# Optimization experiments

Measured on AMD Instinct MI355X. Metric: run time of the kernel, lower is better.

The kernel has to match this reference:

```python
import jax, jax.numpy as jnp
import numpy as np

B, S, HID, NH, KCLIP = 2, 1500, 1024, 16, 64
HD = HID // NH  # 64


def setup_inputs() -> dict:
    key = jax.random.key(0)
    ks = jax.random.split(key, 16)
    std = 0.02
    inp = {
        "query": jax.random.normal(ks[0], (B, S, HID), jnp.float32),
        "key": jax.random.normal(ks[1], (B, S, HID), jnp.float32),
        "value": jax.random.normal(ks[2], (B, S, HID), jnp.float32),
        # per-head projection weights, stacked over heads: [NH, HID, HD]
        "Wq": jax.random.normal(ks[3], (NH, HID, HD), jnp.float32) * std,
        "bq": jax.random.normal(ks[4], (NH, HD), jnp.float32) * std,
        "Wk": jax.random.normal(ks[5], (NH, HID, HD), jnp.float32) * std,
        "bk": jax.random.normal(ks[6], (NH, HD), jnp.float32) * std,
        "Wv": jax.random.normal(ks[7], (NH, HID, HD), jnp.float32) * std,
        "bv": jax.random.normal(ks[8], (NH, HD), jnp.float32) * std,
        # Shaw relative-position embedding tables: [2k+1, HD]
        "pe_k": jax.random.normal(ks[9], (2 * KCLIP + 1, HD), jnp.float32) * std,
        "pe_v": jax.random.normal(ks[10], (2 * KCLIP + 1, HD), jnp.float32) * std,
        # output projection (torch Linear stored as x @ W + b here)
        "W_fc": jax.random.normal(ks[11], (HID, HID), jnp.float32) * std,
        "b_fc": jax.random.normal(ks[12], (HID,), jnp.float32) * std,
    }
    return inp


def _rel_bias(pe, length, k_clip):
    idx = jnp.arange(length)
    dist = jnp.clip(idx[None, :] - idx[:, None], -k_clip, k_clip) + k_clip
    return pe[dist]  # [S, S, HD]


def reference(query, key, value, Wq, bq, Wk, bk, Wv, bv, pe_k, pe_v, W_fc, b_fc):
    head_dim = Wq.shape[-1]
    seq = query.shape[1]
    k_clip = (pe_k.shape[0] - 1) // 2

    kb = _rel_bias(pe_k, seq, k_clip)  # [S, S, HD]
    vb = _rel_bias(pe_v, seq, k_clip)  # [S, S, HD]

    # batched per-head projections: [B, NH, S, HD]
    Q = jnp.einsum('bsh,nhd->bnsd', query, Wq) + bq[None, :, None, :]
    K = jnp.einsum('bsh,nhd->bnsd', key, Wk) + bk[None, :, None, :]
    V = jnp.einsum('bsh,nhd->bnsd', value, Wv) + bv[None, :, None, :]

    # content term + Shaw relative-key bias term
    scores = jnp.einsum('bnqd,bnkd->bnqk', Q, K) \
           + jnp.einsum('bnqd,qkd->bnqk', Q, kb)
    scores = scores / jnp.sqrt(jnp.asarray(head_dim, scores.dtype))

    w = jax.nn.softmax(scores, axis=-1)  # [B, NH, S, S]

    out = jnp.einsum('bnqk,bnkd->bnqd', w, V) \
        + jnp.einsum('bnqk,qkd->bnqd', w, vb)

    # concat heads (head order matches ModuleList concatenation)
    hidden = out.transpose(0, 2, 1, 3).reshape(query.shape[0], seq, -1)
    return hidden @ W_fc + b_fc
```

## Files before the change

### kernel.cpp

```cpp
#include <hip/hip_runtime.h>
#include <math.h>

#define B_     2
#define S_     1500
#define HID_   1024
#define NH_    16
#define HD_    64
#define M_     (B_*S_)
#define SP_    1536
#define LOG2E  1.4426950408889634f

typedef short bf16x8 __attribute__((ext_vector_type(8)));
typedef short bf16x4 __attribute__((ext_vector_type(4)));
typedef float f32x4  __attribute__((ext_vector_type(4)));

__device__ __forceinline__ float b2f(short s) {
    unsigned u = ((unsigned)(unsigned short)s) << 16;
    return __uint_as_float(u);
}
__device__ __forceinline__ short f2b(float f) {
    unsigned u = __float_as_uint(f);
    unsigned r = (u + 0x7FFFu + ((u >> 16) & 1u)) >> 16;
    return (short)r;
}
__device__ __forceinline__ void gload16(const short* src, short* lds) {
    __builtin_amdgcn_global_load_lds(
        (const __attribute__((address_space(1))) void*)src,
        (__attribute__((address_space(3))) void*)lds, 16, 0, 0);
}

__global__ __launch_bounds__(256) void cvt_act3(
    const float* __restrict__ q, const float* __restrict__ k,
    const float* __restrict__ v, short* __restrict__ oq,
    short* __restrict__ ok, short* __restrict__ ov)
{
    const float* src = blockIdx.y == 0 ? q : blockIdx.y == 1 ? k : v;
    short* dst       = blockIdx.y == 0 ? oq : blockIdx.y == 1 ? ok : ov;
    int i = blockIdx.x * 256 + threadIdx.x;
    const float4* p = (const float4*)(src + (size_t)i * 8);
    float4 a = p[0], b = p[1];
    bf16x8 o;
    o[0]=f2b(a.x); o[1]=f2b(a.y); o[2]=f2b(a.z); o[3]=f2b(a.w);
    o[4]=f2b(b.x); o[5]=f2b(b.y); o[6]=f2b(b.z); o[7]=f2b(b.w);
    *(bf16x8*)(dst + (size_t)i * 8) = o;
}

__global__ __launch_bounds__(256) void prep_w(
    const float* __restrict__ Wq, const float* __restrict__ Wk,
    const float* __restrict__ Wv, const float* __restrict__ Wfc,
    const float* __restrict__ pe_k, const float* __restrict__ pe_v,
    short* __restrict__ Wqt, short* __restrict__ Wkt, short* __restrict__ Wvt,
    short* __restrict__ Wfh, short* __restrict__ Wfl,
    short* __restrict__ pe_kb, short* __restrict__ pe_vt)
{
    int z = blockIdx.x, tid = threadIdx.x;
    if (z == 1024) {
        for (int s = tid; s < 144 * 64; s += 256) {
            int j = s >> 6, d = s & 63;
            pe_kb[s] = (j < 129) ? f2b(pe_k[j * 64 + d]) : (short)0;
        }
        for (int s = tid; s < 64 * 160; s += 256) {
            int d = s / 160, j = s - d * 160;
            pe_vt[s] = (j < 129) ? f2b(pe_v[j * 64 + d]) : (short)0;
        }
        return;
    }
    __shared__ float T[64][65];
    const float* src; short* dhi; short* dlo = nullptr;
    int C, c0, r0; float scale = 1.f;
    if (z < 768) {
        int widx = z >> 8, rem = z & 255;
        int h = rem >> 4, rt = rem & 15;
        src = (widx == 0 ? Wq : widx == 1 ? Wk : Wv) + (size_t)h * 1024 * 64;
        dhi = (widx == 0 ? Wqt : widx == 1 ? Wkt : Wvt) + (size_t)h * 64 * 1024;
        scale = (widx == 0) ? 0.125f * LOG2E : 1.0f;
        C = 64; c0 = 0; r0 = rt * 64;
    } else {
        int idx = z - 768;
        src = Wfc; dhi = Wfh; dlo = Wfl;
        C = 1024; c0 = (idx >> 4) * 64; r0 = (idx & 15) * 64;
    }
#pragma unroll
    for (int i = 0; i < 4; ++i) {
        int slot = tid + i * 256;
        int r = slot >> 4, cg = (slot & 15) * 4;
        float4 v = *(const float4*)(src + (size_t)(r0 + r) * C + c0 + cg);
        T[r][cg+0] = v.x*scale; T[r][cg+1] = v.y*scale;
        T[r][cg+2] = v.z*scale; T[r][cg+3] = v.w*scale;
    }
    __syncthreads();
#pragma unroll
    for (int i = 0; i < 16; ++i) {
        int slot = tid + i * 256;
        int c = slot >> 6, r = slot & 63;
        float v = T[r][c];
        short hi = f2b(v);
        size_t o = (size_t)(c0 + c) * 1024 + r0 + r;
        dhi[o] = hi;
        if (dlo) dlo[o] = f2b(v - b2f(hi));
    }
}

__device__ __forceinline__ void gemm_core(
    const short* __restrict__ Ahi, const short* __restrict__ Alo,
    const short* __restrict__ Bhi, const short* __restrict__ Blo,
    int kIters, int m0, int n0, short* As, short* Bs, f32x4 (&acc)[4][4])
{
    const int tid = threadIdx.x, w = tid >> 6, lane = tid & 63;
    const int l15 = lane & 15, lr4 = lane >> 4;
    const int wr = w >> 1, wc = w & 1;

    for (int it = 0; it < kIters; ++it) {
        int kt = it * 64;
        int seg = kt >> 10, kk0 = kt & 1023;
        const short* Aseg = (seg == 1) ? Alo : Ahi;
        const short* Bseg = (seg == 2) ? Blo : Bhi;
        __syncthreads();
#pragma unroll
        for (int c = 0; c < 4; ++c) {
            int slot = (w * 4 + c) * 64 + lane;
            int r = slot >> 3, cb = slot & 7;
            int sm = m0 + r; sm = sm < M_ ? sm : M_ - 1;
            gload16(Aseg + (size_t)sm * 1024 + kk0 + ((cb ^ (r & 7)) * 8),
                    As + (size_t)(w * 4 + c) * 512);
            gload16(Bseg + (size_t)(n0 + r) * 1024 + kk0 + ((cb ^ (r & 7)) * 8),
                    Bs + (size_t)(w * 4 + c) * 512);
        }
        __syncthreads();
#pragma unroll
        for (int kh = 0; kh < 2; ++kh) {
            bf16x8 aF[4], bF[4];
#pragma unroll
            for (int mi = 0; mi < 4; ++mi) {
                int r = wr * 64 + mi * 16 + l15;
                aF[mi] = *(const bf16x8*)(As + r * 64 + (((kh*4+lr4) ^ (r & 7)) * 8));
            }
#pragma unroll
            for (int ni = 0; ni < 4; ++ni) {
                int r = wc * 64 + ni * 16 + l15;
                bF[ni] = *(const bf16x8*)(Bs + r * 64 + (((kh*4+lr4) ^ (r & 7)) * 8));
            }
#pragma unroll
            for (int mi = 0; mi < 4; ++mi)
#pragma unroll
                for (int ni = 0; ni < 4; ++ni)
                    acc[mi][ni] = __builtin_amdgcn_mfma_f32_16x16x32_bf16(
                        aF[mi], bF[ni], acc[mi][ni], 0, 0, 0);
        }
    }
}

__global__ __launch_bounds__(256) void gemm_qkv(
    const short* __restrict__ qb, const short* __restrict__ kb,
    const short* __restrict__ vb, const short* __restrict__ Wqt,
    const short* __restrict__ Wkt, const short* __restrict__ Wvt,
    const float* __restrict__ bq, const float* __restrict__ bk,
    const float* __restrict__ bv,
    short* __restrict__ Qp, short* __restrict__ Kp, short* __restrict__ Vp)
{
    __shared__ short As[128 * 64];
    __shared__ short Bs[128 * 64];
    const int z = blockIdx.z;
    const short* A  = z == 0 ? qb : z == 1 ? kb : vb;
    const short* Bw = z == 0 ? Wqt : z == 1 ? Wkt : Wvt;
    const float* bias = z == 0 ? bq : z == 1 ? bk : bv;
    const float bscale = z == 0 ? 0.125f * LOG2E : 1.0f;
    short* out = z == 0 ? Qp : z == 1 ? Kp : Vp;
    const int m0 = blockIdx.x * 128, n0 = blockIdx.y * 128;

    f32x4 zf = {0.f,0.f,0.f,0.f};
    f32x4 acc[4][4];
#pragma unroll
    for (int i = 0; i < 4; ++i)
#pragma unroll
        for (int j = 0; j < 4; ++j) acc[i][j] = zf;

    gemm_core(A, A, Bw, Bw, 16, m0, n0, As, Bs, acc);

    const int tid = threadIdx.x, w = tid >> 6, lane = tid & 63;
    const int l15 = lane & 15, lr4 = lane >> 4;
    const int wr = w >> 1, wc = w & 1;
#pragma unroll
    for (int mi = 0; mi < 4; ++mi)
#pragma unroll
        for (int rr = 0; rr < 4; ++rr) {
            int m = m0 + wr * 64 + mi * 16 + lr4 * 4 + rr;
            if (m >= M_) continue;
            int b = m / S_, s = m - b * S_;
#pragma unroll
            for (int ni = 0; ni < 4; ++ni) {
                int n = n0 + wc * 64 + ni * 16 + l15;
                float v = acc[mi][ni][rr] + bias[n] * bscale;
                int h = n >> 6, d = n & 63;
                out[(((size_t)(b * NH_ + h)) * S_ + s) * HD_ + d] = f2b(v);
            }
        }
}

__global__ __launch_bounds__(256) void gemm_fc(
    const short* __restrict__ Ahi, const short* __restrict__ Alo,
    const short* __restrict__ Bhi, const short* __restrict__ Blo,
    const float* __restrict__ bias, float* __restrict__ out)
{
    __shared__ short As[128 * 64];
    __shared__ short Bs[128 * 64];
    const int m0 = blockIdx.x * 128, n0 = blockIdx.y * 128;
    f32x4 zf = {0.f,0.f,0.f,0.f};
    f32x4 acc[4][4];
#pragma unroll
    for (int i = 0; i < 4; ++i)
#pragma unroll
        for (int j = 0; j < 4; ++j) acc[i][j] = zf;

    gemm_core(Ahi, Alo, Bhi, Blo, 32, m0, n0, As, Bs, acc);

    const int tid = threadIdx.x, w = tid >> 6, lane = tid & 63;
    const int l15 = lane & 15, lr4 = lane >> 4;
    const int wr = w >> 1, wc = w & 1;
#pragma unroll
    for (int mi = 0; mi < 4; ++mi)
#pragma unroll
        for (int rr = 0; rr < 4; ++rr) {
            int m = m0 + wr * 64 + mi * 16 + lr4 * 4 + rr;
            if (m >= M_) continue;
#pragma unroll
            for (int ni = 0; ni < 4; ++ni) {
                int n = n0 + wc * 64 + ni * 16 + l15;
                out[(size_t)m * 1024 + n] = acc[mi][ni][rr] + bias[n];
            }
        }
}

__global__ __launch_bounds__(256) void vtrans(
    const short* __restrict__ Vp, short* __restrict__ Vtg)
{
    __shared__ short T[64][72];
    const int bh = blockIdx.y, s0 = blockIdx.x * 64, tid = threadIdx.x;
    const size_t kv = (size_t)bh * S_ * 64;
#pragma unroll
    for (int i = 0; i < 2; ++i) {
        int slot = tid + i * 256;
        int r = slot >> 3, cb = slot & 7;
        int ss = s0 + r; ss = ss < S_ ? ss : S_ - 1;
        bf16x8 v = *(const bf16x8*)(Vp + kv + (size_t)ss * 64 + cb * 8);
        *(bf16x8*)(&T[r][cb * 8]) = v;
    }
    __syncthreads();
#pragma unroll
    for (int i = 0; i < 2; ++i) {
        int slot = tid + i * 256;
        int d = slot >> 3, cg = slot & 7;
        bf16x8 v;
#pragma unroll
        for (int j = 0; j < 8; ++j) {
            int kk = 32 * (cg >> 2) + ((j >> 2) & 1) * 16 + (cg & 3) * 4 + (j & 3);
            v[j] = T[kk][d];
        }
        *(bf16x8*)(Vtg + ((size_t)bh * 64 + d) * SP_ + s0 + cg * 8) = v;
    }
}

__global__ __launch_bounds__(256) void attn_mfma(
    const short* __restrict__ Qb, const short* __restrict__ Kb,
    const short* __restrict__ Vtg, const short* __restrict__ pe_kb,
    const short* __restrict__ pe_vt,
    short* __restrict__ hid_hi, short* __restrict__ hid_lo)
{
    __shared__ short Kc[128 * 64];
    __shared__ short Vt[64 * 128];
    __shared__ short qpe[64 * 144];
    __shared__ short wsm[64 * 160];

    const int tid = threadIdx.x, w = tid >> 6, lane = tid & 63;
    const int l15 = lane & 15, lr4 = lane >> 4;
    const int lg = (blockIdx.x & 7) * 96 + (blockIdx.x >> 3);
    const int bh = lg / 24, bx = lg - bh * 24;
    const int q0 = bx * 64;
    const int qw = q0 + w * 16;
    const int myq = qw + l15;
    const int myrow = w * 16 + l15;
    const size_t kv  = (size_t)bh * S_ * HD_;
    const size_t vtb = (size_t)bh * 64 * SP_;

    {
        short ini = f2b(-1e30f);
        bf16x8 iv;
#pragma unroll
        for (int i = 0; i < 8; ++i) iv[i] = ini;
        short* base = wsm + w * 16 * 160;
#pragma unroll
        for (int i = 0; i < 5; ++i)
            *(bf16x8*)(base + (size_t)(i * 64 + lane) * 8) = iv;
    }
#pragma unroll
    for (int cc = 0; cc < 2; ++cc) {
        int slot = (w * 2 + cc) * 64 + lane;
        int r = slot >> 3, cb = slot & 7;
        int sq = q0 + r; sq = sq < S_ ? sq : S_ - 1;
        gload16(Qb + kv + (size_t)sq * 64 + ((cb ^ (r & 7)) * 8),
                Kc + (size_t)(w * 2 + cc) * 512);
    }
    __syncthreads();

    bf16x8 qA[2];
    {
        int r = myrow;
        qA[0] = *(const bf16x8*)(Kc + r * 64 + ((lr4 ^ (r & 7)) * 8));
        qA[1] = *(const bf16x8*)(Kc + r * 64 + (((4 + lr4) ^ (r & 7)) * 8));
    }

    f32x4 zf = {0.f,0.f,0.f,0.f};
#pragma unroll
    for (int jt = 0; jt < 9; ++jt) {
        f32x4 a = zf;
#pragma unroll
        for (int kh = 0; kh < 2; ++kh) {
            bf16x8 pf = *(const bf16x8*)(pe_kb + (size_t)(jt * 16 + l15) * 64 + kh * 32 + lr4 * 8);
            a = __builtin_amdgcn_mfma_f32_16x16x32_bf16(pf, qA[kh], a, 0, 0, 0);
        }
        bf16x4 pk;
#pragma unroll
        for (int rr = 0; rr < 4; ++rr) pk[rr] = f2b(a[rr]);
        *(bf16x4*)(qpe + (size_t)myrow * 144 + jt * 16 + lr4 * 4) = pk;
    }
    const float qpe0   = b2f(qpe[myrow * 144 + 0]);
    const float qpe128 = b2f(qpe[myrow * 144 + 128]);
    __syncthreads();

    float m = -1e30f, s0s = 0.f, s1s = 0.f;
    f32x4 o[4];
#pragma unroll
    for (int t = 0; t < 4; ++t) o[t] = zf;

    for (int c = 0; c < 12; ++c) {
        const int kc = c * 128;
#pragma unroll
        for (int cc = 0; cc < 4; ++cc) {
            int slot = (w * 4 + cc) * 64 + lane;
            int rK = slot >> 3, cbK = slot & 7;
            int sk = kc + rK; sk = sk < S_ ? sk : S_ - 1;
            gload16(Kb + kv + (size_t)sk * 64 + ((cbK ^ (rK & 7)) * 8),
                    Kc + (size_t)(w * 4 + cc) * 512);
            int rV = slot >> 4, cbV = slot & 15;
            gload16(Vtg + vtb + (size_t)rV * SP_ + kc + ((cbV ^ (rV & 7)) * 8),
                    Vt + (size_t)(w * 4 + cc) * 512);
        }
        __syncthreads();

        __builtin_amdgcn_s_setprio(1);
        f32x4 sa[8];
#pragma unroll
        for (int t8 = 0; t8 < 8; ++t8) {
            sa[t8] = zf;
#pragma unroll
            for (int kh = 0; kh < 2; ++kh) {
                int r = t8 * 16 + l15;
                bf16x8 kB = *(const bf16x8*)(Kc + r * 64 + (((kh*4+lr4) ^ (r & 7)) * 8));
                sa[t8] = __builtin_amdgcn_mfma_f32_16x16x32_bf16(kB, qA[kh], sa[t8], 0, 0, 0);
            }
        }
        __builtin_amdgcn_s_setprio(0);

        const bool lo0 = (kc +  63 - qw) <= -64, hi0 = (kc       - (qw + 15)) >= 64;
        const bool lo1 = (kc + 127 - qw) <= -64, hi1 = (kc + 64  - (qw + 15)) >= 64;
        const bool mx0 = !(lo0 || hi0), mx1 = !(lo1 || hi1);
        const float ub0 = lo0 ? qpe0 : qpe128;
        const float ub1 = lo1 ? qpe0 : qpe128;

        float lg2[8][4];
        float rm = -1e30f;
#pragma unroll
        for (int t8 = 0; t8 < 8; ++t8) {
            const bool mx = (t8 < 4) ? mx0 : mx1;
            const float ub = (t8 < 4) ? ub0 : ub1;
#pragma unroll
            for (int rr = 0; rr < 4; ++rr) {
                int k = kc + t8 * 16 + lr4 * 4 + rr;
                int rel = k - myq;
                float v;
                if (mx) {
                    int jc = rel < -64 ? 0 : (rel > 64 ? 128 : rel + 64);
                    v = sa[t8][rr] + b2f(qpe[myrow * 144 + jc]);
                } else {
                    v = sa[t8][rr] + ub;
                }
                if (k >= S_) v = -1e30f;
                lg2[t8][rr] = v;
                rm = fmaxf(rm, v);
                if (mx && rel > -64 && rel < 64)
                    wsm[myrow * 160 + rel + 64] = f2b(v);
            }
        }
        rm = fmaxf(rm, __shfl_xor(rm, 16));
        rm = fmaxf(rm, __shfl_xor(rm, 32));

        if (!__all(rm <= m + 8.f)) {
            float nm = fmaxf(m, rm);
            float fac = exp2f(m - nm);
            m = nm; s0s *= fac; s1s *= fac;
            float fo[4];
#pragma unroll
            for (int rr = 0; rr < 4; ++rr) fo[rr] = __shfl(fac, lr4 * 4 + rr);
#pragma unroll
            for (int t = 0; t < 4; ++t)
#pragma unroll
                for (int rr = 0; rr < 4; ++rr) o[t][rr] *= fo[rr];
        }

        bf16x8 pa[2][2];
        float ls0 = 0.f, ls1 = 0.f;
#pragma unroll
        for (int t8 = 0; t8 < 8; ++t8) {
            const int h = t8 >> 2, tt = t8 & 3;
            const int wn = tt >> 1, sl = (tt & 1) * 4;
            const bool mx = h ? mx1 : mx0;
            const bool alo = h ? lo1 : lo0;
#pragma unroll
            for (int rr = 0; rr < 4; ++rr) {
                float p2 = exp2f(lg2[t8][rr] - m);
                pa[h][wn][sl + rr] = f2b(p2);
                if (mx) {
                    int rel = (kc + t8 * 16 + lr4 * 4 + rr) - myq;
                    if (rel <= -64) ls0 += p2; else if (rel >= 64) ls1 += p2;
                } else if (alo) ls0 += p2; else ls1 += p2;
            }
        }
        ls0 += __shfl_xor(ls0, 16); ls0 += __shfl_xor(ls0, 32);
        ls1 += __shfl_xor(ls1, 16); ls1 += __shfl_xor(ls1, 32);
        s0s += ls0; s1s += ls1;

        __builtin_amdgcn_s_setprio(1);
#pragma unroll
        for (int h = 0; h < 2; ++h)
#pragma unroll
            for (int wn = 0; wn < 2; ++wn)
#pragma unroll
                for (int td = 0; td < 4; ++td) {
                    int r = td * 16 + l15;
                    int cbv = h * 8 + wn * 4 + lr4;
                    bf16x8 vB = *(const bf16x8*)(Vt + r * 128 + ((cbv ^ (r & 7)) * 8));
                    o[td] = __builtin_amdgcn_mfma_f32_16x16x32_bf16(pa[h][wn], vB, o[td], 0, 0, 0);
                }
        __builtin_amdgcn_s_setprio(0);

        __syncthreads();
    }

    short* rowp = wsm + (size_t)myrow * 160;
    float midsum = 0.f;
#pragma unroll
    for (int cc = 0; cc < 5; ++cc) {
        int off = (cc * 4 + lr4) * 8;
        bf16x8 mv = *(const bf16x8*)(rowp + off);
        bf16x8 ev;
#pragma unroll
        for (int jj = 0; jj < 8; ++jj) {
            float e = exp2f(b2f(mv[jj]) - m);
            ev[jj] = f2b(e);
            midsum += e;
        }
        *(bf16x8*)(rowp + off) = ev;
    }
    midsum += __shfl_xor(midsum, 16); midsum += __shfl_xor(midsum, 32);
    const float linv = 1.f / (s0s + s1s + midsum);
    if (lr4 == 0) { rowp[0] = f2b(s0s); rowp[128] = f2b(s1s); }

#pragma unroll
    for (int jh = 0; jh < 5; ++jh) {
        bf16x8 aW = *(const bf16x8*)(wsm + (size_t)myrow * 160 + jh * 32 + lr4 * 8);
#pragma unroll
        for (int td = 0; td < 4; ++td) {
            bf16x8 bW = *(const bf16x8*)(pe_vt + (size_t)(td * 16 + l15) * 160 + jh * 32 + lr4 * 8);
            o[td] = __builtin_amdgcn_mfma_f32_16x16x32_bf16(aW, bW, o[td], 0, 0, 0);
        }
    }

    {
        float fo[4];
#pragma unroll
        for (int rr = 0; rr < 4; ++rr) fo[rr] = __shfl(linv, lr4 * 4 + rr);
#pragma unroll
        for (int td = 0; td < 4; ++td)
#pragma unroll
            for (int rr = 0; rr < 4; ++rr) o[td][rr] *= fo[rr];
    }

#pragma unroll
    for (int td = 0; td < 4; ++td)
#pragma unroll
        for (int rr = 0; rr < 4; ++rr) {
            int qrow = lr4 * 4 + rr;
            int d = td * 16 + l15;
            int inner = (((d >> 2) ^ ((qrow & 7) << 1)) << 2) + (d & 3);
            float v = o[td][rr];
            short hi = f2b(v);
            wsm[(w * 16 + qrow) * 160 + inner] = hi;
            qpe[(w * 16 + qrow) * 144 + inner] = f2b(v - b2f(hi));
        }
    {
        int b = bh >> 4, h = bh & 15;
        int qrow = lane >> 2;
        int q = q0 + w * 16 + qrow;
#pragma unroll
        for (int i = 0; i < 2; ++i) {
            int cb = (lane & 3) * 2 + i;
            int qws = (cb * 2) ^ ((qrow & 7) << 1);
            bf16x8 hv = *(const bf16x8*)(wsm + (w * 16 + qrow) * 160 + qws * 4);
            bf16x8 lv = *(const bf16x8*)(qpe + (w * 16 + qrow) * 144 + qws * 4);
            if (q < S_) {
                size_t oo = ((size_t)(b * S_ + q)) * 1024 + h * 64 + cb * 8;
                *(bf16x8*)(hid_hi + oo) = hv;
                *(bf16x8*)(hid_lo + oo) = lv;
            }
        }
    }
}

extern "C" void kernel_launch(void* const* d_in, const int* in_sizes, int n_in,
                              void* d_out, int out_size, void* d_ws, size_t ws_size,
                              hipStream_t stream)
{
    const float* query = (const float*)d_in[0];
    const float* key   = (const float*)d_in[1];
    const float* value = (const float*)d_in[2];
    const float* Wq    = (const float*)d_in[3];
    const float* bq    = (const float*)d_in[4];
    const float* Wk    = (const float*)d_in[5];
    const float* bk    = (const float*)d_in[6];
    const float* Wv    = (const float*)d_in[7];
    const float* bv    = (const float*)d_in[8];
    const float* pe_k  = (const float*)d_in[9];
    const float* pe_v  = (const float*)d_in[10];
    const float* W_fc  = (const float*)d_in[11];
    const float* b_fc  = (const float*)d_in[12];

    char* W = (char*)d_ws;
    short* qb   = (short*)(W + 0);
    short* kb   = (short*)(W + 6291456);
    short* vb   = (short*)(W + 12582912);
    short* Vtg  = vb;
    short* Wqt  = (short*)(W + 18874368);
    short* Wkt  = (short*)(W + 20971520);
    short* Wvt  = (short*)(W + 23068672);
    short* Wfh  = (short*)(W + 25165824);
    short* Wfl  = (short*)(W + 27262976);
    short* Qp   = (short*)(W + 29360128);
    short* Kp   = (short*)(W + 35651584);
    short* Vp   = (short*)(W + 41943040);
    short* pekb = (short*)(W + 48234496);
    short* pevt = (short*)(W + 48252928);
    short* hidh = qb;
    short* hidl = kb;

    cvt_act3<<<dim3(1500, 3), 256, 0, stream>>>(query, key, value, qb, kb, vb);
    prep_w<<<1025, 256, 0, stream>>>(Wq, Wk, Wv, W_fc, pe_k, pe_v,
                                     Wqt, Wkt, Wvt, Wfh, Wfl, pekb, pevt);
    gemm_qkv<<<dim3(24, 8, 3), 256, 0, stream>>>(qb, kb, vb, Wqt, Wkt, Wvt,
                                                 bq, bk, bv, Qp, Kp, Vp);
    vtrans<<<dim3(24, 32), 256, 0, stream>>>(Vp, Vtg);
    attn_mfma<<<768, 256, 0, stream>>>(Qp, Kp, Vtg, pekb, pevt, hidh, hidl);
    gemm_fc<<<dim3(24, 8), 256, 0, stream>>>(hidh, hidl, Wfh, Wfl, b_fc, (float*)d_out);
}
```

Measured before the change: 260.6 us.

## Fuse QK MFMA with exponentiation using a deferred running max

The QK^T MFMAs are merged into the softmax loop, so each 16-key tile's scores are exponentiated right away against the previous running max. The max update and rescaling of the output accumulator now happen after the PV MFMAs, and the running max starts at 0 instead of -inf. The cross-lane shuffle reductions of the partial sums move out of the chunk loop to a single reduction at the end. This is meant to cut the sa/lg2 register arrays and the shuffle work done per chunk. The cost is that exp2 is taken with a stale max, which can overflow if a chunk's scores jump far above the current max.

```diff
diff --git a/kernel.cpp b/kernel.cpp
--- a/kernel.cpp
+++ b/kernel.cpp
@@ -327,7 +327,7 @@
     const float qpe128 = b2f(qpe[myrow * 144 + 128]);
     __syncthreads();
 
-    float m = -1e30f, s0s = 0.f, s1s = 0.f;
+    float m = 0.f, s0s = 0.f, s1s = 0.f;
     f32x4 o[4];
 #pragma unroll
     for (int t = 0; t < 4; ++t) o[t] = zf;
@@ -347,32 +347,28 @@
         }
         __syncthreads();
 
-        __builtin_amdgcn_s_setprio(1);
-        f32x4 sa[8];
-#pragma unroll
-        for (int t8 = 0; t8 < 8; ++t8) {
-            sa[t8] = zf;
-#pragma unroll
-            for (int kh = 0; kh < 2; ++kh) {
-                int r = t8 * 16 + l15;
-                bf16x8 kB = *(const bf16x8*)(Kc + r * 64 + (((kh*4+lr4) ^ (r & 7)) * 8));
-                sa[t8] = __builtin_amdgcn_mfma_f32_16x16x32_bf16(kB, qA[kh], sa[t8], 0, 0, 0);
-            }
-        }
-        __builtin_amdgcn_s_setprio(0);
-
         const bool lo0 = (kc +  63 - qw) <= -64, hi0 = (kc       - (qw + 15)) >= 64;
         const bool lo1 = (kc + 127 - qw) <= -64, hi1 = (kc + 64  - (qw + 15)) >= 64;
         const bool mx0 = !(lo0 || hi0), mx1 = !(lo1 || hi1);
         const float ub0 = lo0 ? qpe0 : qpe128;
         const float ub1 = lo1 ? qpe0 : qpe128;
 
-        float lg2[8][4];
         float rm = -1e30f;
+        bf16x8 pa[2][2];
 #pragma unroll
         for (int t8 = 0; t8 < 8; ++t8) {
-            const bool mx = (t8 < 4) ? mx0 : mx1;
-            const float ub = (t8 < 4) ? ub0 : ub1;
+            f32x4 s = zf;
+#pragma unroll
+            for (int kh = 0; kh < 2; ++kh) {
+                int r = t8 * 16 + l15;
+                bf16x8 kB = *(const bf16x8*)(Kc + r * 64 + (((kh*4+lr4) ^ (r & 7)) * 8));
+                s = __builtin_amdgcn_mfma_f32_16x16x32_bf16(kB, qA[kh], s, 0, 0, 0);
+            }
+            const int h = t8 >> 2, tt = t8 & 3;
+            const int wn = tt >> 1, sl = (tt & 1) * 4;
+            const bool mx = h ? mx1 : mx0;
+            const bool alo = h ? lo1 : lo0;
+            const float ub = h ? ub1 : ub0;
 #pragma unroll
             for (int rr = 0; rr < 4; ++rr) {
                 int k = kc + t8 * 16 + lr4 * 4 + rr;
@@ -380,54 +376,21 @@
                 float v;
                 if (mx) {
                     int jc = rel < -64 ? 0 : (rel > 64 ? 128 : rel + 64);
-                    v = sa[t8][rr] + b2f(qpe[myrow * 144 + jc]);
+                    v = s[rr] + b2f(qpe[myrow * 144 + jc]);
                 } else {
-                    v = sa[t8][rr] + ub;
+                    v = s[rr] + ub;
                 }
                 if (k >= S_) v = -1e30f;
-                lg2[t8][rr] = v;
                 rm = fmaxf(rm, v);
                 if (mx && rel > -64 && rel < 64)
                     wsm[myrow * 160 + rel + 64] = f2b(v);
-            }
-        }
-        rm = fmaxf(rm, __shfl_xor(rm, 16));
-        rm = fmaxf(rm, __shfl_xor(rm, 32));
-
-        if (!__all(rm <= m + 8.f)) {
-            float nm = fmaxf(m, rm);
-            float fac = exp2f(m - nm);
-            m = nm; s0s *= fac; s1s *= fac;
-            float fo[4];
-#pragma unroll
-            for (int rr = 0; rr < 4; ++rr) fo[rr] = __shfl(fac, lr4 * 4 + rr);
-#pragma unroll
-            for (int t = 0; t < 4; ++t)
-#pragma unroll
-                for (int rr = 0; rr < 4; ++rr) o[t][rr] *= fo[rr];
-        }
-
-        bf16x8 pa[2][2];
-        float ls0 = 0.f, ls1 = 0.f;
-#pragma unroll
-        for (int t8 = 0; t8 < 8; ++t8) {
-            const int h = t8 >> 2, tt = t8 & 3;
-            const int wn = tt >> 1, sl = (tt & 1) * 4;
-            const bool mx = h ? mx1 : mx0;
-            const bool alo = h ? lo1 : lo0;
-#pragma unroll
-            for (int rr = 0; rr < 4; ++rr) {
-                float p2 = exp2f(lg2[t8][rr] - m);
+                float p2 = exp2f(v - m);
                 pa[h][wn][sl + rr] = f2b(p2);
                 if (mx) {
-                    int rel = (kc + t8 * 16 + lr4 * 4 + rr) - myq;
-                    if (rel <= -64) ls0 += p2; else if (rel >= 64) ls1 += p2;
-                } else if (alo) ls0 += p2; else ls1 += p2;
-            }
-        }
-        ls0 += __shfl_xor(ls0, 16); ls0 += __shfl_xor(ls0, 32);
-        ls1 += __shfl_xor(ls1, 16); ls1 += __shfl_xor(ls1, 32);
-        s0s += ls0; s1s += ls1;
+                    if (rel <= -64) s0s += p2; else if (rel >= 64) s1s += p2;
+                } else if (alo) s0s += p2; else s1s += p2;
+            }
+        }
 
         __builtin_amdgcn_s_setprio(1);
 #pragma unroll
@@ -443,8 +406,26 @@
                 }
         __builtin_amdgcn_s_setprio(0);
 
+        rm = fmaxf(rm, __shfl_xor(rm, 16));
+        rm = fmaxf(rm, __shfl_xor(rm, 32));
+        if (!__all(rm <= m + 8.f)) {
+            float nm = fmaxf(m, rm);
+            float fac = exp2f(m - nm);
+            m = nm; s0s *= fac; s1s *= fac;
+            float fo[4];
+#pragma unroll
+            for (int rr = 0; rr < 4; ++rr) fo[rr] = __shfl(fac, lr4 * 4 + rr);
+#pragma unroll
+            for (int t = 0; t < 4; ++t)
+#pragma unroll
+                for (int rr = 0; rr < 4; ++rr) o[t][rr] *= fo[rr];
+        }
+
         __syncthreads();
     }
+
+    s0s += __shfl_xor(s0s, 16); s0s += __shfl_xor(s0s, 32);
+    s1s += __shfl_xor(s1s, 16); s1s += __shfl_xor(s1s, 32);
 
     short* rowp = wsm + (size_t)myrow * 160;
     float midsum = 0.f;
```

After: 262.7 us. Within noise of the previous version (+0.8%).
